# Optimization experiments

Measured on AMD Instinct MI355X. Metric: run time of the kernel, lower is better.

Reference implementation:

```python
import jax, jax.numpy as jnp
import numpy as np
from jax import lax

B, DIM, H, W = 4, 128, 128, 128
HEADS = 8
HID = int(DIM * 2.66)  # 340, IEL hidden_features
EPS_LN = 1e-6


def conv(x, w, b=None, groups=1, pad=0):
    out = lax.conv_general_dilated(
        x, w, (1, 1), [(pad, pad), (pad, pad)],
        feature_group_count=groups,
        dimension_numbers=('NCHW', 'OIHW', 'NCHW'))
    if b is not None:
        out = out + b[None, :, None, None]
    return out


def setup_inputs() -> dict:
    key = jax.random.key(0)
    ks = jax.random.split(key, 16)
    def wgt(k, shape, s=0.05):
        return jax.random.normal(k, shape, jnp.float32) * s
    return dict(
        x=jax.random.normal(ks[0], (B, DIM, H, W), jnp.float32),
        y=jax.random.normal(ks[1], (B, DIM, H, W), jnp.float32),
        ln_w=jnp.ones((DIM,), jnp.float32),
        ln_b=jnp.zeros((DIM,), jnp.float32),
        temperature=jnp.ones((HEADS, 1, 1), jnp.float32),
        q_w=wgt(ks[2], (DIM, DIM, 1, 1)),
        qdw_w=wgt(ks[3], (DIM, 1, 3, 3)),
        kv_w=wgt(ks[4], (2 * DIM, DIM, 1, 1)),
        kvdw_w=wgt(ks[5], (2 * DIM, 1, 3, 3)),
        po_w=wgt(ks[6], (DIM, DIM, 1, 1)),
        g1_w=wgt(ks[7], (DIM // 2, DIM, 1, 1)),
        g1_b=jnp.zeros((DIM // 2,), jnp.float32),
        g2_w=wgt(ks[8], (1, DIM // 2, 1, 1)),
        g2_b=jnp.zeros((1,), jnp.float32),
        pin_w=wgt(ks[9], (2 * HID, DIM, 1, 1)),
        dw_w=wgt(ks[10], (2 * HID, 1, 3, 3)),
        dw1_w=wgt(ks[11], (HID, 1, 3, 3)),
        dw2_w=wgt(ks[12], (HID, 1, 3, 3)),
        pout_w=wgt(ks[13], (DIM, HID, 1, 1)),
    )


def reference(x, y, ln_w, ln_b, temperature, q_w, qdw_w, kv_w, kvdw_w, po_w,
              g1_w, g1_b, g2_w, g2_b, pin_w, dw_w, dw1_w, dw2_w, pout_w):
    Bn, C, Hh, Ww = x.shape
    ch = C // HEADS  # channel tokens per head

    def ln(z):  # channels_first LayerNorm over channel axis
        u = z.mean(1, keepdims=True)
        s = ((z - u) ** 2).mean(1, keepdims=True)
        return ln_w[None, :, None, None] * ((z - u) / jnp.sqrt(s + EPS_LN)) + ln_b[None, :, None, None]

    xn = ln(x)
    yn = ln(y)

    # SCAB: transposed (channel) attention with dynamic top-k mask
    q = conv(conv(xn, q_w), qdw_w, groups=C, pad=1)
    kv = conv(conv(yn, kv_w), kvdw_w, groups=2 * C, pad=1)
    k, v = jnp.split(kv, 2, axis=1)
    q = q.reshape(Bn, HEADS, ch, Hh * Ww)
    k = k.reshape(Bn, HEADS, ch, Hh * Ww)
    v = v.reshape(Bn, HEADS, ch, Hh * Ww)
    q = q / jnp.maximum(jnp.linalg.norm(q, axis=-1, keepdims=True), 1e-12)
    k = k / jnp.maximum(jnp.linalg.norm(k, axis=-1, keepdims=True), 1e-12)

    # gate -> dynamic_k = int(ch * mean(gate)) as in torch (truncation)
    g = jax.nn.sigmoid(conv(jax.nn.relu(conv(xn, g1_w, g1_b)), g2_w, g2_b))
    dk = jnp.clip((ch * lax.stop_gradient(g).mean()).astype(jnp.int32), 1, ch)

    attn = jnp.einsum('bhcn,bhdn->bhcd', q, k) * temperature[None]  # [B,H,ch,ch]
    order = jnp.argsort(-attn, axis=-1)       # topk ordering (descending)
    ranks = jnp.argsort(order, axis=-1)       # rank of each entry in its row
    attn = jnp.where(ranks < dk, attn, -jnp.inf)
    attn = jax.nn.softmax(attn, axis=-1)
    out = jnp.einsum('bhcd,bhdn->bhcn', attn, v).reshape(Bn, C, Hh, Ww)
    x = x + conv(out, po_w)

    # IEL: tanh-gated dwconv FFN
    z = ln(x)
    t = conv(conv(z, pin_w), dw_w, groups=2 * HID, pad=1)
    x1, x2 = jnp.split(t, 2, axis=1)
    x1 = jnp.tanh(conv(x1, dw1_w, groups=HID, pad=1)) + x1
    x2 = jnp.tanh(conv(x2, dw2_w, groups=HID, pad=1)) + x2
    return conv(x1 * x2, pout_w) + x
```

## Files before the change

kernel.cpp:

```cpp
#include <hip/hip_runtime.h>
#include <math.h>

static constexpr int Bn    = 4;
static constexpr int Cc    = 128;
static constexpr int Hh    = 128;
static constexpr int Wb    = 128;
static constexpr int Nn    = Hh * Wb;
static constexpr int HEADS = 8;
static constexpr int CHh   = 16;
static constexpr int HID   = 340;
static constexpr int HID2  = 680;
static constexpr int NS    = 64;
static constexpr int MPAD  = 704;
static constexpr int KPAD2 = 352;

typedef unsigned short ushort_t;
typedef __attribute__((ext_vector_type(8))) short short8;
typedef __attribute__((ext_vector_type(4))) float f32x4;

__device__ __forceinline__ ushort_t f2bf(float f) {
    unsigned u = __float_as_uint(f);
    return (ushort_t)((u + 0x7FFFu + ((u >> 16) & 1u)) >> 16);
}
__device__ __forceinline__ float bf2f(ushort_t h) {
    return __uint_as_float(((unsigned)h) << 16);
}

__global__ __launch_bounds__(256) void ln_kernel(const float* __restrict__ in,
                                                 const float* __restrict__ w,
                                                 const float* __restrict__ bias,
                                                 float* __restrict__ out) {
    int p = blockIdx.x * 256 + threadIdx.x;
    int b = blockIdx.z;
    const float* ib = in + (size_t)b * Cc * Nn + p;
    float s = 0.f, s2 = 0.f;
    #pragma unroll 8
    for (int c = 0; c < Cc; ++c) {
        float v = ib[(size_t)c * Nn];
        s += v; s2 += v * v;
    }
    float mean = s * (1.0f / Cc);
    float var  = s2 * (1.0f / Cc) - mean * mean;
    float inv  = 1.0f / sqrtf(var + 1e-6f);
    float* ob = out + (size_t)b * Cc * Nn + p;
    #pragma unroll 8
    for (int c = 0; c < Cc; ++c) {
        float v = ib[(size_t)c * Nn];
        ob[(size_t)c * Nn] = w[c] * ((v - mean) * inv) + bias[c];
    }
}

__global__ __launch_bounds__(256) void ln_bf16_kernel(const float* __restrict__ in,
                                                      const float* __restrict__ w,
                                                      const float* __restrict__ bias,
                                                      ushort_t* __restrict__ out) {
    int p = blockIdx.x * 256 + threadIdx.x;
    int b = blockIdx.z;
    const float* ib = in + (size_t)b * Cc * Nn + p;
    float s = 0.f, s2 = 0.f;
    #pragma unroll 8
    for (int c = 0; c < Cc; ++c) {
        float v = ib[(size_t)c * Nn];
        s += v; s2 += v * v;
    }
    float mean = s * (1.0f / Cc);
    float var  = s2 * (1.0f / Cc) - mean * mean;
    float inv  = 1.0f / sqrtf(var + 1e-6f);
    ushort_t* ob = out + (size_t)b * Cc * Nn + p;
    #pragma unroll 8
    for (int c = 0; c < Cc; ++c) {
        float v = ib[(size_t)c * Nn];
        ob[(size_t)c * Nn] = f2bf(w[c] * ((v - mean) * inv) + bias[c]);
    }
}

__global__ __launch_bounds__(256) void wconv_pad_rows_kernel(const float* __restrict__ w,
                                                             ushort_t* __restrict__ o,
                                                             int rows, int K) {
    int idx = blockIdx.x * 256 + threadIdx.x;
    int r = idx / K, k = idx - r * K;
    o[idx] = (r < rows) ? f2bf(w[(size_t)r * K + k]) : (ushort_t)0;
}
__global__ __launch_bounds__(256) void wconv_pad_cols_kernel(const float* __restrict__ w,
                                                             ushort_t* __restrict__ o,
                                                             int K, int Kp) {
    int idx = blockIdx.x * 256 + threadIdx.x;
    int r = idx / Kp, k = idx - r * Kp;
    o[idx] = (k < K) ? f2bf(w[(size_t)r * K + k]) : (ushort_t)0;
}

__global__ __launch_bounds__(256) void gemm_bf16_kernel(const ushort_t* __restrict__ Zh,
                                                        const ushort_t* __restrict__ Wh,
                                                        const float* __restrict__ bias,
                                                        const float* __restrict__ res,
                                                        float* outf,
                                                        ushort_t* outh,
                                                        int Cin, int Kpad, int Mreal,
                                                        int act) {
    const int b    = blockIdx.z;
    const int px0  = blockIdx.x * 128;
    const int co0  = blockIdx.y * 64;
    const int tid  = threadIdx.x;
    const int wv   = tid >> 6;
    const int lane = tid & 63;
    const int n    = lane & 15;
    const int q    = lane >> 4;

    __shared__ ushort_t Bl[128][40];

    const ushort_t* Zb = Zh + (size_t)b * Cin * Nn;

    f32x4 acc[4][2];
    #pragma unroll
    for (int i = 0; i < 4; ++i)
        #pragma unroll
        for (int j = 0; j < 2; ++j) acc[i][j] = (f32x4){0.f, 0.f, 0.f, 0.f};

    for (int k0 = 0; k0 < Kpad; k0 += 32) {
        {
            int r = tid >> 3;
            int s = tid & 7;
            int ci = k0 + r;
            ushort_t tmp[16];
            if (ci < Cin) {
                const ushort_t* src = Zb + (size_t)ci * Nn + px0 + s * 16;
                uint4 v0 = *(const uint4*)src;
                uint4 v1 = *(const uint4*)(src + 8);
                tmp[0]  = (ushort_t)(v0.x & 0xFFFF); tmp[1]  = (ushort_t)(v0.x >> 16);
                tmp[2]  = (ushort_t)(v0.y & 0xFFFF); tmp[3]  = (ushort_t)(v0.y >> 16);
                tmp[4]  = (ushort_t)(v0.z & 0xFFFF); tmp[5]  = (ushort_t)(v0.z >> 16);
                tmp[6]  = (ushort_t)(v0.w & 0xFFFF); tmp[7]  = (ushort_t)(v0.w >> 16);
                tmp[8]  = (ushort_t)(v1.x & 0xFFFF); tmp[9]  = (ushort_t)(v1.x >> 16);
                tmp[10] = (ushort_t)(v1.y & 0xFFFF); tmp[11] = (ushort_t)(v1.y >> 16);
                tmp[12] = (ushort_t)(v1.z & 0xFFFF); tmp[13] = (ushort_t)(v1.z >> 16);
                tmp[14] = (ushort_t)(v1.w & 0xFFFF); tmp[15] = (ushort_t)(v1.w >> 16);
            } else {
                #pragma unroll
                for (int i = 0; i < 16; ++i) tmp[i] = 0;
            }
            #pragma unroll
            for (int i = 0; i < 16; ++i) Bl[s * 16 + i][r] = tmp[i];
        }
        __syncthreads();

        short8 bfrag[2];
        #pragma unroll
        for (int px16 = 0; px16 < 2; ++px16)
            bfrag[px16] = *(const short8*)&Bl[wv * 32 + px16 * 16 + n][q * 8];
        #pragma unroll
        for (int mt = 0; mt < 4; ++mt) {
            const ushort_t* wp = Wh + (size_t)(co0 + mt * 16 + n) * Kpad + k0 + q * 8;
            short8 afrag = *(const short8*)wp;
            #pragma unroll
            for (int px16 = 0; px16 < 2; ++px16)
                acc[mt][px16] = __builtin_amdgcn_mfma_f32_16x16x32_bf16(
                    afrag, bfrag[px16], acc[mt][px16], 0, 0, 0);
        }
        __syncthreads();
    }

    #pragma unroll
    for (int px16 = 0; px16 < 2; ++px16) {
        int px = px0 + wv * 32 + px16 * 16 + n;
        #pragma unroll
        for (int mt = 0; mt < 4; ++mt) {
            #pragma unroll
            for (int reg = 0; reg < 4; ++reg) {
                int co = co0 + mt * 16 + q * 4 + reg;
                if (co < Mreal) {
                    float v = acc[mt][px16][reg];
                    if (bias) v += bias[co];
                    if (act == 1) v = fmaxf(v, 0.f);
                    size_t o = ((size_t)b * Mreal + co) * Nn + px;
                    if (res)  v += res[o];
                    if (outf) outf[o] = v;
                    if (outh) outh[o] = f2bf(v);
                }
            }
        }
    }
}

template <int TCO>
__global__ __launch_bounds__(256) void conv1x1v_kernel(const float* __restrict__ in,
                                                       const float* __restrict__ wgt,
                                                       int wstride,
                                                       const float* __restrict__ bias,
                                                       const float* __restrict__ res,
                                                       float* __restrict__ out,
                                                       int Cin, int Cout, int act) {
    int pg  = blockIdx.x * 256 + threadIdx.x;
    int b   = blockIdx.z;
    int co0 = blockIdx.y * TCO;

    const float* wrow[TCO];
    #pragma unroll
    for (int i = 0; i < TCO; ++i) {
        int co = co0 + i; if (co > Cout - 1) co = Cout - 1;
        wrow[i] = wgt + (size_t)co * wstride;
    }

    float4 acc[TCO];
    #pragma unroll
    for (int i = 0; i < TCO; ++i) acc[i] = make_float4(0.f, 0.f, 0.f, 0.f);

    const float* ib = in + (size_t)b * Cin * Nn + (size_t)pg * 4;
    #pragma unroll 8
    for (int ci = 0; ci < Cin; ++ci) {
        float4 v = *(const float4*)(ib + (size_t)ci * Nn);
        #pragma unroll
        for (int i = 0; i < TCO; ++i) {
            float w = wrow[i][ci];
            acc[i].x += v.x * w; acc[i].y += v.y * w;
            acc[i].z += v.z * w; acc[i].w += v.w * w;
        }
    }

    #pragma unroll
    for (int i = 0; i < TCO; ++i) {
        int co = co0 + i;
        if (co < Cout) {
            float4 r = acc[i];
            if (bias) { float bb = bias[co]; r.x += bb; r.y += bb; r.z += bb; r.w += bb; }
            if (act == 1) {
                r.x = fmaxf(r.x, 0.f); r.y = fmaxf(r.y, 0.f);
                r.z = fmaxf(r.z, 0.f); r.w = fmaxf(r.w, 0.f);
            }
            size_t o = ((size_t)b * Cout + co) * Nn + (size_t)pg * 4;
            if (res) {
                float4 rv = *(const float4*)(res + o);
                r.x += rv.x; r.y += rv.y; r.z += rv.z; r.w += rv.w;
            }
            *(float4*)(out + o) = r;
        }
    }
}

__global__ __launch_bounds__(256) void dw3x3_kernel(const float* __restrict__ in,
                                                    const float* __restrict__ w,
                                                    float* __restrict__ out, int Ct) {
    int p = blockIdx.x * 256 + threadIdx.x;
    int c = blockIdx.y;
    int b = blockIdx.z;
    int y = p >> 7, x = p & (Wb - 1);
    const float* ib = in + ((size_t)b * Ct + c) * Nn;
    float wl[9];
    #pragma unroll
    for (int k = 0; k < 9; ++k) wl[k] = w[c * 9 + k];
    float acc = 0.f;
    #pragma unroll
    for (int dy = 0; dy < 3; ++dy) {
        int yy = y + dy - 1;
        if (yy < 0 || yy >= Hh) continue;
        #pragma unroll
        for (int dx = 0; dx < 3; ++dx) {
            int xx = x + dx - 1;
            if (xx < 0 || xx >= Wb) continue;
            acc += wl[dy * 3 + dx] * ib[yy * Wb + xx];
        }
    }
    out[((size_t)b * Ct + c) * Nn + p] = acc;
}

__global__ __launch_bounds__(256) void dw3x3_bf16_kernel(const ushort_t* __restrict__ in,
                                                         const float* __restrict__ w,
                                                         float* __restrict__ out, int Ct) {
    int p = blockIdx.x * 256 + threadIdx.x;
    int c = blockIdx.y;
    int b = blockIdx.z;
    int y = p >> 7, x = p & (Wb - 1);
    const ushort_t* ib = in + ((size_t)b * Ct + c) * Nn;
    float wl[9];
    #pragma unroll
    for (int k = 0; k < 9; ++k) wl[k] = w[c * 9 + k];
    float acc = 0.f;
    #pragma unroll
    for (int dy = 0; dy < 3; ++dy) {
        int yy = y + dy - 1;
        if (yy < 0 || yy >= Hh) continue;
        #pragma unroll
        for (int dx = 0; dx < 3; ++dx) {
            int xx = x + dx - 1;
            if (xx < 0 || xx >= Wb) continue;
            acc += wl[dy * 3 + dx] * bf2f(ib[yy * Wb + xx]);
        }
    }
    out[((size_t)b * Ct + c) * Nn + p] = acc;
}

__global__ __launch_bounds__(256) void l2norm_kernel(float* __restrict__ data, int cstride) {
    int b = blockIdx.z, c = blockIdx.x;
    float* ptr = data + ((size_t)b * cstride + c) * Nn;
    int t = threadIdx.x;
    float s = 0.f;
    for (int i = t; i < Nn; i += 256) { float v = ptr[i]; s += v * v; }
    __shared__ float red[256];
    red[t] = s; __syncthreads();
    for (int st = 128; st > 0; st >>= 1) { if (t < st) red[t] += red[t + st]; __syncthreads(); }
    float scale = 1.0f / fmaxf(sqrtf(red[0]), 1e-12f);
    for (int i = t; i < Nn; i += 256) ptr[i] *= scale;
}

__global__ __launch_bounds__(256) void gate2_kernel(const float* __restrict__ gmid,
                                                    const float* __restrict__ w2,
                                                    const float* __restrict__ b2,
                                                    float* __restrict__ blocksums,
                                                    int out_off) {
    int p = blockIdx.x * 256 + threadIdx.x;
    int b = blockIdx.z;
    float acc = b2[0];
    const float* ib = gmid + (size_t)b * 64 * Nn + p;
    #pragma unroll 8
    for (int ci = 0; ci < 64; ++ci) acc += ib[(size_t)ci * Nn] * w2[ci];
    float g = 1.0f / (1.0f + expf(-acc));
    __shared__ float red[256];
    int t = threadIdx.x;
    red[t] = g; __syncthreads();
    for (int st = 128; st > 0; st >>= 1) { if (t < st) red[t] += red[t + st]; __syncthreads(); }
    if (t == 0) blocksums[out_off + b * 64 + blockIdx.x] = red[0];
}

__global__ __launch_bounds__(256) void gate_final_kernel(const float* __restrict__ blocksums,
                                                         int* __restrict__ dk_out) {
    __shared__ double sred[256];
    int t = threadIdx.x;
    sred[t] = (double)blocksums[t];
    __syncthreads();
    for (int st = 128; st > 0; st >>= 1) { if (t < st) sred[t] += sred[t + st]; __syncthreads(); }
    if (t == 0) {
        double mean = sred[0] / (double)(Bn * Nn);
        float val = 16.0f * (float)mean;
        int dk = (int)val;
        if (dk < 1) dk = 1;
        if (dk > 16) dk = 16;
        *dk_out = dk;
    }
}

__global__ __launch_bounds__(256) void attn_qk_partial_kernel(const float* __restrict__ q,
                                                              const float* __restrict__ k,
                                                              int kstride,
                                                              float* __restrict__ partial) {
    int ns = blockIdx.x, h = blockIdx.y, b = blockIdx.z;
    int t = threadIdx.x;
    int c = t >> 4, d = t & 15;
    __shared__ float qs[16][65];
    __shared__ float ks[16][65];
    const float* qb = q + ((size_t)b * Cc + h * CHh) * Nn;
    const float* kb = k + ((size_t)b * kstride + h * CHh) * Nn;
    float acc = 0.f;
    int nbeg = ns * (Nn / NS);
    for (int n0 = nbeg; n0 < nbeg + (Nn / NS); n0 += 64) {
        for (int idx = t; idx < 1024; idx += 256) {
            int r = idx >> 6, col = idx & 63;
            qs[r][col] = qb[(size_t)r * Nn + n0 + col];
            ks[r][col] = kb[(size_t)r * Nn + n0 + col];
        }
        __syncthreads();
        #pragma unroll
        for (int j = 0; j < 64; ++j) acc += qs[c][j] * ks[d][j];
        __syncthreads();
    }
    partial[(((size_t)(b * HEADS + h)) * NS + ns) * 256 + t] = acc;
}

__global__ __launch_bounds__(256) void attn_reduce_kernel(const float* __restrict__ partial,
                                                          const float* __restrict__ temp,
                                                          float* __restrict__ attnp) {
    int bh = blockIdx.x;
    int h = bh % HEADS;
    int t = threadIdx.x;
    const float* pp = partial + (size_t)bh * NS * 256 + t;
    float s = 0.f;
    #pragma unroll 8
    for (int ns = 0; ns < NS; ++ns) s += pp[(size_t)ns * 256];
    attnp[(size_t)bh * 256 + t] = s * temp[h];
}

__global__ void topk_softmax_kernel(float* __restrict__ attnp, const int* __restrict__ dkp) {
    int bh = blockIdx.x;
    int c = threadIdx.x;
    if (c >= 16) return;
    float* row = attnp + ((size_t)bh * CHh + c) * CHh;
    float a[16];
    #pragma unroll
    for (int d = 0; d < 16; ++d) a[d] = row[d];
    int dk = *dkp;
    unsigned keep = 0;
    float m = -INFINITY;
    #pragma unroll
    for (int d = 0; d < 16; ++d) {
        int rank = 0;
        #pragma unroll
        for (int j = 0; j < 16; ++j)
            rank += (a[j] > a[d]) || (a[j] == a[d] && j < d);
        if (rank < dk) { keep |= (1u << d); m = fmaxf(m, a[d]); }
    }
    float e[16]; float s = 0.f;
    #pragma unroll
    for (int d = 0; d < 16; ++d) {
        e[d] = (keep >> d & 1u) ? expf(a[d] - m) : 0.f;
        s += e[d];
    }
    float invs = 1.0f / s;
    #pragma unroll
    for (int d = 0; d < 16; ++d) row[d] = e[d] * invs;
}

__global__ __launch_bounds__(256) void attn_v_kernel(const float* __restrict__ attnp,
                                                     const float* __restrict__ v,
                                                     float* __restrict__ out) {
    int p = blockIdx.x * 256 + threadIdx.x;
    int cg = blockIdx.y;
    int b = blockIdx.z;
    int h = cg >> 4, cr = cg & 15;
    const float* arow = attnp + (((size_t)b * HEADS + h) * CHh + cr) * CHh;
    const float* vb = v + ((size_t)b * Cc + h * CHh) * Nn + p;
    float acc = 0.f;
    #pragma unroll
    for (int d = 0; d < 16; ++d) acc += arow[d] * vb[(size_t)d * Nn];
    out[((size_t)b * Cc + cg) * Nn + p] = acc;
}

__global__ __launch_bounds__(256) void attn_v_bf16_kernel(const float* __restrict__ attnp,
                                                          const float* __restrict__ v,
                                                          int vstride, int voff,
                                                          ushort_t* __restrict__ out) {
    int p = blockIdx.x * 256 + threadIdx.x;
    int cg = blockIdx.y;
    int b = blockIdx.z;
    int h = cg >> 4, cr = cg & 15;
    const float* arow = attnp + (((size_t)b * HEADS + h) * CHh + cr) * CHh;
    const float* vb = v + ((size_t)b * vstride + voff + h * CHh) * Nn + p;
    float acc = 0.f;
    #pragma unroll
    for (int d = 0; d < 16; ++d) acc += arow[d] * vb[(size_t)d * Nn];
    out[((size_t)b * Cc + cg) * Nn + p] = f2bf(acc);
}

__global__ __launch_bounds__(256) void iel_tail_v4_kernel(const ushort_t* __restrict__ Th,
                                                          const float* __restrict__ dww,
                                                          const float* __restrict__ dw1p,
                                                          const float* __restrict__ dw2p,
                                                          ushort_t* __restrict__ PRh) {
    const int gy0 = blockIdx.x * 16;
    const int c   = blockIdx.y;
    const int b   = blockIdx.z;
    const int tid = threadIdx.x;

    __shared__ float ts[2][20][132];
    __shared__ float us[2][18][132];

    const ushort_t* t1 = Th + ((size_t)b * HID2 + c) * Nn;
    const ushort_t* t2 = Th + ((size_t)b * HID2 + HID + c) * Nn;

    for (int idx = tid; idx < 640; idx += 256) {
        int ti  = idx / 320;
        int rem = idx - ti * 320;
        int i   = rem >> 4;
        int seg = rem & 15;
        int gy  = gy0 - 2 + i;
        const ushort_t* tp = ti ? t2 : t1;
        float vals[8];
        if (gy >= 0 && gy < Hh) {
            uint4 v = *(const uint4*)(tp + gy * Wb + seg * 8);
            vals[0] = bf2f((ushort_t)(v.x & 0xFFFF)); vals[1] = bf2f((ushort_t)(v.x >> 16));
            vals[2] = bf2f((ushort_t)(v.y & 0xFFFF)); vals[3] = bf2f((ushort_t)(v.y >> 16));
            vals[4] = bf2f((ushort_t)(v.z & 0xFFFF)); vals[5] = bf2f((ushort_t)(v.z >> 16));
            vals[6] = bf2f((ushort_t)(v.w & 0xFFFF)); vals[7] = bf2f((ushort_t)(v.w >> 16));
        } else {
            #pragma unroll
            for (int k = 0; k < 8; ++k) vals[k] = 0.f;
        }
        #pragma unroll
        for (int k = 0; k < 8; ++k) ts[ti][i][1 + seg * 8 + k] = vals[k];
        if (seg == 0)  ts[ti][i][0] = 0.f;
        if (seg == 15) { ts[ti][i][129] = 0.f; ts[ti][i][130] = 0.f; ts[ti][i][131] = 0.f; }
    }
    __syncthreads();

    float wA[9], wB[9], w1[9], w2[9];
    #pragma unroll
    for (int k = 0; k < 9; ++k) {
        wA[k] = dww[c * 9 + k];
        wB[k] = dww[(HID + c) * 9 + k];
        w1[k] = dw1p[c * 9 + k];
        w2[k] = dw2p[c * 9 + k];
    }

    for (int idx = tid; idx < 1152; idx += 256) {
        int ti  = idx / 576;
        int rem = idx - ti * 576;
        int i   = rem >> 5;
        int s   = rem & 31;
        int gy  = gy0 - 1 + i;
        float o0 = 0.f, o1 = 0.f, o2 = 0.f, o3 = 0.f;
        if (gy >= 0 && gy < Hh) {
            const float* wp = ti ? wB : wA;
            #pragma unroll
            for (int dy = 0; dy < 3; ++dy) {
                const float* row = &ts[ti][i + dy][4 * s];
                float4 a = *(const float4*)row;
                float2 bb = *(const float2*)(row + 4);
                float w0 = wp[dy * 3 + 0], w1t = wp[dy * 3 + 1], w2t = wp[dy * 3 + 2];
                o0 += w0 * a.x + w1t * a.y + w2t * a.z;
                o1 += w0 * a.y + w1t * a.z + w2t * a.w;
                o2 += w0 * a.z + w1t * a.w + w2t * bb.x;
                o3 += w0 * a.w + w1t * bb.x + w2t * bb.y;
            }
        }
        int j0 = 1 + 4 * s;
        us[ti][i][j0]     = o0;
        us[ti][i][j0 + 1] = o1;
        us[ti][i][j0 + 2] = o2;
        us[ti][i][j0 + 3] = o3;
    }
    if (tid < 72) {
        int ti = tid / 36;
        int r  = tid - ti * 36;
        int i  = r >> 1;
        us[ti][i][(r & 1) ? 129 : 0] = 0.f;
    }
    __syncthreads();

    ushort_t* outp = PRh + ((size_t)b * HID + c) * Nn;
    for (int idx = tid; idx < 512; idx += 256) {
        int r  = idx >> 5;
        int s  = idx & 31;
        int x0 = 4 * s;
        float s1a[4] = {0.f, 0.f, 0.f, 0.f};
        float s2a[4] = {0.f, 0.f, 0.f, 0.f};
        float c1a[4], c2a[4];
        #pragma unroll
        for (int dy = 0; dy < 3; ++dy) {
            const float* r0 = &us[0][r + dy][x0];
            float4 a0 = *(const float4*)r0;
            float2 b0 = *(const float2*)(r0 + 4);
            const float* r1 = &us[1][r + dy][x0];
            float4 a1 = *(const float4*)r1;
            float2 b1 = *(const float2*)(r1 + 4);
            float w10 = w1[dy * 3], w11 = w1[dy * 3 + 1], w12 = w1[dy * 3 + 2];
            float w20 = w2[dy * 3], w21 = w2[dy * 3 + 1], w22 = w2[dy * 3 + 2];
            s1a[0] += w10 * a0.x + w11 * a0.y + w12 * a0.z;
            s1a[1] += w10 * a0.y + w11 * a0.z + w12 * a0.w;
            s1a[2] += w10 * a0.z + w11 * a0.w + w12 * b0.x;
            s1a[3] += w10 * a0.w + w11 * b0.x + w12 * b0.y;
            s2a[0] += w20 * a1.x + w21 * a1.y + w22 * a1.z;
            s2a[1] += w20 * a1.y + w21 * a1.z + w22 * a1.w;
            s2a[2] += w20 * a1.z + w21 * a1.w + w22 * b1.x;
            s2a[3] += w20 * a1.w + w21 * b1.x + w22 * b1.y;
            if (dy == 1) {
                c1a[0] = a0.y; c1a[1] = a0.z; c1a[2] = a0.w; c1a[3] = b0.x;
                c2a[0] = a1.y; c2a[1] = a1.z; c2a[2] = a1.w; c2a[3] = b1.x;
            }
        }
        uint2 pk;
        float v0 = (tanhf(s1a[0]) + c1a[0]) * (tanhf(s2a[0]) + c2a[0]);
        float v1 = (tanhf(s1a[1]) + c1a[1]) * (tanhf(s2a[1]) + c2a[1]);
        float v2 = (tanhf(s1a[2]) + c1a[2]) * (tanhf(s2a[2]) + c2a[2]);
        float v3 = (tanhf(s1a[3]) + c1a[3]) * (tanhf(s2a[3]) + c2a[3]);
        pk.x = (unsigned)f2bf(v0) | ((unsigned)f2bf(v1) << 16);
        pk.y = (unsigned)f2bf(v2) | ((unsigned)f2bf(v3) << 16);
        *(uint2*)(outp + (gy0 + r) * Wb + x0) = pk;
    }
}

__global__ __launch_bounds__(256) void iel_tail_f32_kernel(const float* __restrict__ t1p,
                                                           const float* __restrict__ t2p,
                                                           const float* __restrict__ dwA,
                                                           const float* __restrict__ dwB,
                                                           const float* __restrict__ dw1p,
                                                           const float* __restrict__ dw2p,
                                                           float* __restrict__ prod) {
    const int c = blockIdx.y;
    const int tilesx = Wb / 16;
    const int ty0 = (blockIdx.x / tilesx) * 16;
    const int tx0 = (blockIdx.x % tilesx) * 16;
    const int tid = threadIdx.x;

    __shared__ float ts[2][20][24];
    __shared__ float us[2][18][24];

    const float* t1 = t1p + (size_t)c * Nn;
    const float* t2 = t2p + (size_t)c * Nn;

    for (int idx = tid; idx < 400; idx += 256) {
        int i = idx / 20, j = idx % 20;
        int gy = ty0 - 2 + i, gx = tx0 - 2 + j;
        bool ok = (gy >= 0 && gy < Hh && gx >= 0 && gx < Wb);
        ts[0][i][j] = ok ? t1[gy * Wb + gx] : 0.f;
        ts[1][i][j] = ok ? t2[gy * Wb + gx] : 0.f;
    }
    __syncthreads();

    float wA[9], wB[9], w1[9], w2[9];
    #pragma unroll
    for (int k = 0; k < 9; ++k) {
        wA[k] = dwA[c * 9 + k];
        wB[k] = dwB[c * 9 + k];
        w1[k] = dw1p[c * 9 + k];
        w2[k] = dw2p[c * 9 + k];
    }

    for (int idx = tid; idx < 324; idx += 256) {
        int i = idx / 18, j = idx % 18;
        int gy = ty0 - 1 + i, gx = tx0 - 1 + j;
        float a0 = 0.f, a1 = 0.f;
        if (gy >= 0 && gy < Hh && gx >= 0 && gx < Wb) {
            #pragma unroll
            for (int dy = 0; dy < 3; ++dy)
                #pragma unroll
                for (int dx = 0; dx < 3; ++dx) {
                    a0 += wA[dy * 3 + dx] * ts[0][i + dy][j + dx];
                    a1 += wB[dy * 3 + dx] * ts[1][i + dy][j + dx];
                }
        }
        us[0][i][j] = a0;
        us[1][i][j] = a1;
    }
    __syncthreads();

    int ty = tid >> 4, tx = tid & 15;
    float c1 = us[0][ty + 1][tx + 1];
    float c2 = us[1][ty + 1][tx + 1];
    float s1 = 0.f, s2 = 0.f;
    #pragma unroll
    for (int dy = 0; dy < 3; ++dy)
        #pragma unroll
        for (int dx = 0; dx < 3; ++dx) {
            s1 += w1[dy * 3 + dx] * us[0][ty + dy][tx + dx];
            s2 += w2[dy * 3 + dx] * us[1][ty + dy][tx + dx];
        }
    float x1t = tanhf(s1) + c1;
    float x2t = tanhf(s2) + c2;
    prod[(size_t)c * Nn + (ty0 + ty) * Wb + (tx0 + tx)] = x1t * x2t;
}

extern "C" void kernel_launch(void* const* d_in, const int* in_sizes, int n_in,
                              void* d_out, int out_size, void* d_ws, size_t ws_size,
                              hipStream_t stream) {
    const float* x      = (const float*)d_in[0];
    const float* y      = (const float*)d_in[1];
    const float* ln_w   = (const float*)d_in[2];
    const float* ln_b   = (const float*)d_in[3];
    const float* temp   = (const float*)d_in[4];
    const float* q_w    = (const float*)d_in[5];
    const float* qdw_w  = (const float*)d_in[6];
    const float* kv_w   = (const float*)d_in[7];
    const float* kvdw_w = (const float*)d_in[8];
    const float* po_w   = (const float*)d_in[9];
    const float* g1_w   = (const float*)d_in[10];
    const float* g1_b   = (const float*)d_in[11];
    const float* g2_w   = (const float*)d_in[12];
    const float* g2_b   = (const float*)d_in[13];
    const float* pin_w  = (const float*)d_in[14];
    const float* dw_w   = (const float*)d_in[15];
    const float* dw1_w  = (const float*)d_in[16];
    const float* dw2_w  = (const float*)d_in[17];
    const float* pout_w = (const float*)d_in[18];
    float* out = (float*)d_out;

    char* ws = (char*)d_ws;
    float* attn      = (float*)ws;
    float* blocksums = (float*)(ws + 32768);
    int*   dk        = (int*)(ws + 33792);
    ushort_t* qWh  = (ushort_t*)(ws + 34816);
    ushort_t* kvWh = qWh + 16384;
    ushort_t* poWh = kvWh + 32768;
    ushort_t* g1Wh = poWh + 16384;
    ushort_t* Wh1  = g1Wh + 8192;
    ushort_t* Wh2  = Wh1 + (size_t)MPAD * Cc;
    float* pool    = (float*)(ws + (1u << 20));

    const size_t CN    = (size_t)Cc * Nn;
    const size_t SLOT1 = (size_t)Bn * CN;
    const size_t TIER1_NEED = 65536 + 6 * SLOT1 * 4;

    dim3 blk(256);
    const int PGX = Nn / 1024;

    if (ws_size >= TIER1_NEED) {
        float* S3 = pool;
        float* S4 = pool + 8 * 1024 * 1024;
        ushort_t* XNh  = (ushort_t*)(pool + 24 * 1024 * 1024);
        ushort_t* YNh  = XNh + Bn * CN;
        ushort_t* KV1h = YNh + Bn * CN;
        ushort_t* Q1h  = KV1h + 2 * Bn * CN;
        float* gmid    = (float*)Q1h;
        float* partial = gmid;
        ushort_t* AOh  = XNh;

        wconv_pad_rows_kernel<<<dim3(64), blk, 0, stream>>>(q_w, qWh, 128, Cc);
        wconv_pad_rows_kernel<<<dim3(128), blk, 0, stream>>>(kv_w, kvWh, 256, Cc);
        wconv_pad_rows_kernel<<<dim3(64), blk, 0, stream>>>(po_w, poWh, 128, Cc);
        wconv_pad_rows_kernel<<<dim3(32), blk, 0, stream>>>(g1_w, g1Wh, 64, Cc);
        wconv_pad_rows_kernel<<<dim3(MPAD * Cc / 256), blk, 0, stream>>>(pin_w, Wh1, HID2, Cc);
        wconv_pad_cols_kernel<<<dim3(Cc * KPAD2 / 256), blk, 0, stream>>>(pout_w, Wh2, HID, KPAD2);

        ln_bf16_kernel<<<dim3(Nn / 256, 1, Bn), blk, 0, stream>>>(x, ln_w, ln_b, XNh);
        ln_bf16_kernel<<<dim3(Nn / 256, 1, Bn), blk, 0, stream>>>(y, ln_w, ln_b, YNh);

        gemm_bf16_kernel<<<dim3(Nn / 128, 2, Bn), blk, 0, stream>>>(
            XNh, qWh, nullptr, nullptr, nullptr, Q1h, Cc, Cc, Cc, 0);
        dw3x3_bf16_kernel<<<dim3(Nn / 256, Cc, Bn), blk, 0, stream>>>(Q1h, qdw_w, S3, Cc);

        gemm_bf16_kernel<<<dim3(Nn / 128, 4, Bn), blk, 0, stream>>>(
            YNh, kvWh, nullptr, nullptr, nullptr, KV1h, Cc, Cc, 2 * Cc, 0);
        dw3x3_bf16_kernel<<<dim3(Nn / 256, 2 * Cc, Bn), blk, 0, stream>>>(KV1h, kvdw_w, S4, 2 * Cc);

        gemm_bf16_kernel<<<dim3(Nn / 128, 1, Bn), blk, 0, stream>>>(
            XNh, g1Wh, g1_b, nullptr, gmid, nullptr, Cc, Cc, 64, 1);
        gate2_kernel<<<dim3(Nn / 256, 1, Bn), blk, 0, stream>>>(gmid, g2_w, g2_b, blocksums, 0);
        gate_final_kernel<<<dim3(1), blk, 0, stream>>>(blocksums, dk);

        l2norm_kernel<<<dim3(Cc, 1, Bn), blk, 0, stream>>>(S3, Cc);
        l2norm_kernel<<<dim3(Cc, 1, Bn), blk, 0, stream>>>(S4, 2 * Cc);

        attn_qk_partial_kernel<<<dim3(NS, HEADS, Bn), blk, 0, stream>>>(S3, S4, 2 * Cc, partial);
        attn_reduce_kernel<<<dim3(Bn * HEADS), blk, 0, stream>>>(partial, temp, attn);
        topk_softmax_kernel<<<dim3(Bn * HEADS), dim3(16), 0, stream>>>(attn, dk);
        attn_v_bf16_kernel<<<dim3(Nn / 256, Cc, Bn), blk, 0, stream>>>(
            attn, S4, 2 * Cc, Cc, AOh);

        gemm_bf16_kernel<<<dim3(Nn / 128, 2, Bn), blk, 0, stream>>>(
            AOh, poWh, nullptr, x, out, nullptr, Cc, Cc, Cc, 0);

        ushort_t* ZNh = (ushort_t*)pool;
        ushort_t* Th  = ZNh + Bn * CN;
        ushort_t* PRh = Th + (size_t)Bn * HID2 * Nn;

        ln_bf16_kernel<<<dim3(Nn / 256, 1, Bn), blk, 0, stream>>>(out, ln_w, ln_b, ZNh);

        gemm_bf16_kernel<<<dim3(Nn / 128, MPAD / 64, Bn), blk, 0, stream>>>(
            ZNh, Wh1, nullptr, nullptr, nullptr, Th, Cc, Cc, HID2, 0);

        iel_tail_v4_kernel<<<dim3(Hh / 16, HID, Bn), blk, 0, stream>>>(
            Th, dw_w, dw1_w, dw2_w, PRh);

        gemm_bf16_kernel<<<dim3(Nn / 128, 2, Bn), blk, 0, stream>>>(
            PRh, Wh2, nullptr, out, out, nullptr, HID, KPAD2, Cc, 0);
    } else {
        float* s0 = pool;
        float* s1 = pool + 1 * CN;
        float* s2 = pool + 2 * CN;
        float* s3 = pool + 3 * CN;
        float* s4 = pool + 4 * CN;
        float* s5 = pool + 5 * CN;

        for (int b = 0; b < Bn; ++b) {
            const float* xb = x + (size_t)b * CN;
            ln_kernel<<<dim3(Nn / 256, 1, 1), blk, 0, stream>>>(xb, ln_w, ln_b, s0);
            conv1x1v_kernel<4><<<dim3(PGX, 16, 1), blk, 0, stream>>>(
                s0, g1_w, Cc, g1_b, nullptr, s1, Cc, 64, 1);
            gate2_kernel<<<dim3(Nn / 256, 1, 1), blk, 0, stream>>>(
                s1, g2_w, g2_b, blocksums, b * 64);
        }
        gate_final_kernel<<<dim3(1), blk, 0, stream>>>(blocksums, dk);

        for (int b = 0; b < Bn; ++b) {
            const float* xb = x + (size_t)b * CN;
            const float* yb = y + (size_t)b * CN;
            float* outb = out + (size_t)b * CN;
            float* attnb = attn + (size_t)b * HEADS * CHh * CHh;

            ln_kernel<<<dim3(Nn / 256, 1, 1), blk, 0, stream>>>(xb, ln_w, ln_b, s0);
            ln_kernel<<<dim3(Nn / 256, 1, 1), blk, 0, stream>>>(yb, ln_w, ln_b, s1);

            conv1x1v_kernel<8><<<dim3(PGX, 16, 1), blk, 0, stream>>>(
                s0, q_w, Cc, nullptr, nullptr, s2, Cc, Cc, 0);
            dw3x3_kernel<<<dim3(Nn / 256, Cc, 1), blk, 0, stream>>>(s2, qdw_w, s3, Cc);
            l2norm_kernel<<<dim3(Cc, 1, 1), blk, 0, stream>>>(s3, Cc);

            conv1x1v_kernel<8><<<dim3(PGX, 16, 1), blk, 0, stream>>>(
                s1, kv_w, Cc, nullptr, nullptr, s2, Cc, Cc, 0);
            dw3x3_kernel<<<dim3(Nn / 256, Cc, 1), blk, 0, stream>>>(s2, kvdw_w, s4, Cc);
            l2norm_kernel<<<dim3(Cc, 1, 1), blk, 0, stream>>>(s4, Cc);

            conv1x1v_kernel<8><<<dim3(PGX, 16, 1), blk, 0, stream>>>(
                s1, kv_w + 128 * 128, Cc, nullptr, nullptr, s2, Cc, Cc, 0);
            dw3x3_kernel<<<dim3(Nn / 256, Cc, 1), blk, 0, stream>>>(s2, kvdw_w + 128 * 9, s5, Cc);

            attn_qk_partial_kernel<<<dim3(NS, HEADS, 1), blk, 0, stream>>>(s3, s4, Cc, s2);
            attn_reduce_kernel<<<dim3(HEADS), blk, 0, stream>>>(s2, temp, attnb);
            topk_softmax_kernel<<<dim3(HEADS), dim3(16), 0, stream>>>(attnb, dk);
            attn_v_kernel<<<dim3(Nn / 256, Cc, 1), blk, 0, stream>>>(attnb, s5, s2);

            conv1x1v_kernel<8><<<dim3(PGX, 16, 1), blk, 0, stream>>>(
                s2, po_w, Cc, nullptr, xb, outb, Cc, Cc, 0);
        }

        const int CHUNK = 170;
        const size_t TCH = (size_t)CHUNK * Nn;
        float* zn   = pool;
        float* T1   = pool + CN;
        float* T2   = T1 + TCH;
        float* prod = T2 + TCH;
        for (int b = 0; b < Bn; ++b) {
            float* outb = out + (size_t)b * CN;
            ln_kernel<<<dim3(Nn / 256, 1, 1), blk, 0, stream>>>(outb, ln_w, ln_b, zn);
            for (int c0 = 0; c0 < HID; c0 += CHUNK) {
                conv1x1v_kernel<20><<<dim3(PGX, 9, 1), blk, 0, stream>>>(
                    zn, pin_w + (size_t)c0 * Cc, Cc, nullptr, nullptr, T1, Cc, CHUNK, 0);
                conv1x1v_kernel<20><<<dim3(PGX, 9, 1), blk, 0, stream>>>(
                    zn, pin_w + (size_t)(HID + c0) * Cc, Cc, nullptr, nullptr, T2, Cc, CHUNK, 0);
                iel_tail_f32_kernel<<<dim3(64, CHUNK, 1), blk, 0, stream>>>(
                    T1, T2, dw_w + c0 * 9, dw_w + (HID + c0) * 9,
                    dw1_w + c0 * 9, dw2_w + c0 * 9, prod);
                conv1x1v_kernel<8><<<dim3(PGX, 16, 1), blk, 0, stream>>>(
                    prod, pout_w + c0, HID, nullptr, outb, outb, CHUNK, Cc, 0);
            }
        }
    }
}
```

Baseline: 719.0 us.

## Fold L2 normalization into dwconv sum-of-squares and rescale attention logits

The depthwise 3x3 conv for q and kv is rewritten to stage rows in shared memory, produce four outputs per thread with vector stores, and accumulate per-channel sums of squares through atomics. The two separate l2norm passes over q and k are removed; the norms are applied instead as a scale on the 16x16 attention logits in the reduce kernel. The IEL tail also swaps tanhf for a fast exp/rcp tanh. The cost is atomic float accumulation, which is order-dependent, and slightly lower tanh accuracy.

```diff
diff --git a/kernel.cpp b/kernel.cpp
--- a/kernel.cpp
+++ b/kernel.cpp
@@ -26,6 +26,38 @@
     return __uint_as_float(((unsigned)h) << 16);
 }
 
+__device__ __forceinline__ float fast_tanh(float x) {
+    float a = fabsf(x);
+    a = fminf(a, 12.0f);
+    float e = __expf(2.0f * a);
+    float r = 1.0f - 2.0f * __builtin_amdgcn_rcpf(e + 1.0f);
+    return x < 0.0f ? -r : r;
+}
+
+__device__ __forceinline__ void iel7_stage(float (*ts)[136], const ushort_t* __restrict__ tp,
+                                           int gy0, int tid) {
+    for (int idx = tid; idx < 640; idx += 256) {
+        int i = idx >> 5;
+        int s = idx & 31;
+        int gy = gy0 - 2 + i;
+        float4 v; v.x = 0.f; v.y = 0.f; v.z = 0.f; v.w = 0.f;
+        if (gy >= 0 && gy < Hh) {
+            uint2 u = *(const uint2*)(tp + gy * Wb + 4 * s);
+            v.x = bf2f((ushort_t)(u.x & 0xFFFF)); v.y = bf2f((ushort_t)(u.x >> 16));
+            v.z = bf2f((ushort_t)(u.y & 0xFFFF)); v.w = bf2f((ushort_t)(u.y >> 16));
+        }
+        *(float4*)&ts[i][4 + 4 * s] = v;
+        if (s == 0) {
+            float4 z; z.x = 0.f; z.y = 0.f; z.z = 0.f; z.w = 0.f;
+            *(float4*)&ts[i][0] = z;
+        }
+        if (s == 31) {
+            float4 z; z.x = 0.f; z.y = 0.f; z.z = 0.f; z.w = 0.f;
+            *(float4*)&ts[i][132] = z;
+        }
+    }
+}
+
 __global__ __launch_bounds__(256) void ln_kernel(const float* __restrict__ in,
                                                  const float* __restrict__ w,
                                                  const float* __restrict__ bias,
@@ -87,6 +119,11 @@
     int idx = blockIdx.x * 256 + threadIdx.x;
     int r = idx / Kp, k = idx - r * Kp;
     o[idx] = (k < K) ? f2bf(w[(size_t)r * K + k]) : (ushort_t)0;
+}
+
+__global__ __launch_bounds__(256) void zero_f32_kernel(float* __restrict__ p, int n) {
+    int i = blockIdx.x * 256 + threadIdx.x;
+    if (i < n) p[i] = 0.f;
 }
 
 __global__ __launch_bounds__(256) void gemm_bf16_kernel(const ushort_t* __restrict__ Zh,
@@ -262,30 +299,57 @@
     out[((size_t)b * Ct + c) * Nn + p] = acc;
 }
 
-__global__ __launch_bounds__(256) void dw3x3_bf16_kernel(const ushort_t* __restrict__ in,
-                                                         const float* __restrict__ w,
-                                                         float* __restrict__ out, int Ct) {
-    int p = blockIdx.x * 256 + threadIdx.x;
-    int c = blockIdx.y;
-    int b = blockIdx.z;
-    int y = p >> 7, x = p & (Wb - 1);
+__global__ __launch_bounds__(256) void dw3x3_bf16_v3_kernel(const ushort_t* __restrict__ in,
+                                                            const float* __restrict__ w,
+                                                            float* __restrict__ out, int Ct,
+                                                            float* __restrict__ ssq,
+                                                            int nrmC) {
+    const int gy0 = blockIdx.x * 16;
+    const int c   = blockIdx.y;
+    const int b   = blockIdx.z;
+    const int tid = threadIdx.x;
+
+    __shared__ float ts[20][136];
+
     const ushort_t* ib = in + ((size_t)b * Ct + c) * Nn;
+    iel7_stage(ts, ib, gy0, tid);
+    __syncthreads();
+
     float wl[9];
     #pragma unroll
     for (int k = 0; k < 9; ++k) wl[k] = w[c * 9 + k];
-    float acc = 0.f;
-    #pragma unroll
-    for (int dy = 0; dy < 3; ++dy) {
-        int yy = y + dy - 1;
-        if (yy < 0 || yy >= Hh) continue;
-        #pragma unroll
-        for (int dx = 0; dx < 3; ++dx) {
-            int xx = x + dx - 1;
-            if (xx < 0 || xx >= Wb) continue;
-            acc += wl[dy * 3 + dx] * bf2f(ib[yy * Wb + xx]);
-        }
-    }
-    out[((size_t)b * Ct + c) * Nn + p] = acc;
+
+    float* ob = out + ((size_t)b * Ct + c) * Nn;
+    float s2sum = 0.f;
+    #pragma unroll
+    for (int it = 0; it < 2; ++it) {
+        int idx = tid + it * 256;
+        int r = idx >> 5;
+        int s = idx & 31;
+        float a[4] = {0.f, 0.f, 0.f, 0.f};
+        #pragma unroll
+        for (int dy = 0; dy < 3; ++dy) {
+            const float* row = &ts[r + 1 + dy][4 * s];
+            float4 e0 = *(const float4*)row;
+            float4 e1 = *(const float4*)(row + 4);
+            float4 e2 = *(const float4*)(row + 8);
+            float e[12] = {e0.x, e0.y, e0.z, e0.w, e1.x, e1.y, e1.z, e1.w,
+                           e2.x, e2.y, e2.z, e2.w};
+            float w0 = wl[dy * 3], w1 = wl[dy * 3 + 1], w2 = wl[dy * 3 + 2];
+            #pragma unroll
+            for (int p = 0; p < 4; ++p)
+                a[p] += w0 * e[p + 3] + w1 * e[p + 4] + w2 * e[p + 5];
+        }
+        float4 st; st.x = a[0]; st.y = a[1]; st.z = a[2]; st.w = a[3];
+        *(float4*)(ob + (gy0 + r) * Wb + 4 * s) = st;
+        s2sum += a[0] * a[0] + a[1] * a[1] + a[2] * a[2] + a[3] * a[3];
+    }
+
+    if (ssq != nullptr && c < nrmC) {
+        #pragma unroll
+        for (int o = 32; o > 0; o >>= 1) s2sum += __shfl_xor(s2sum, o, 64);
+        if ((tid & 63) == 0) atomicAdd(&ssq[(size_t)b * nrmC + c], s2sum);
+    }
 }
 
 __global__ __launch_bounds__(256) void l2norm_kernel(float* __restrict__ data, int cstride) {
@@ -320,8 +384,8 @@
     if (t == 0) blocksums[out_off + b * 64 + blockIdx.x] = red[0];
 }
 
-__global__ __launch_bounds__(256) void gate_final_kernel(const float* __restrict__ blocksums,
-                                                         int* __restrict__ dk_out) {
+__global__ void gate_final_kernel(const float* __restrict__ blocksums,
+                                  int* __restrict__ dk_out) {
     __shared__ double sred[256];
     int t = threadIdx.x;
     sred[t] = (double)blocksums[t];
@@ -366,6 +430,8 @@
 
 __global__ __launch_bounds__(256) void attn_reduce_kernel(const float* __restrict__ partial,
                                                           const float* __restrict__ temp,
+                                                          const float* __restrict__ qss,
+                                                          const float* __restrict__ kss,
                                                           float* __restrict__ attnp) {
     int bh = blockIdx.x;
     int h = bh % HEADS;
@@ -374,7 +440,16 @@
     float s = 0.f;
     #pragma unroll 8
     for (int ns = 0; ns < NS; ++ns) s += pp[(size_t)ns * 256];
-    attnp[(size_t)bh * 256 + t] = s * temp[h];
+    float scale = temp[h];
+    if (qss != nullptr) {
+        int b  = bh / HEADS;
+        int cQ = h * CHh + (t >> 4);
+        int cK = h * CHh + (t & 15);
+        float nq = fmaxf(sqrtf(qss[(size_t)b * Cc + cQ]), 1e-12f);
+        float nk = fmaxf(sqrtf(kss[(size_t)b * Cc + cK]), 1e-12f);
+        scale = scale / (nq * nk);
+    }
+    attnp[(size_t)bh * 256 + t] = s * scale;
 }
 
 __global__ void topk_softmax_kernel(float* __restrict__ attnp, const int* __restrict__ dkp) {
@@ -555,10 +630,10 @@
             }
         }
         uint2 pk;
-        float v0 = (tanhf(s1a[0]) + c1a[0]) * (tanhf(s2a[0]) + c2a[0]);
-        float v1 = (tanhf(s1a[1]) + c1a[1]) * (tanhf(s2a[1]) + c2a[1]);
-        float v2 = (tanhf(s1a[2]) + c1a[2]) * (tanhf(s2a[2]) + c2a[2]);
-        float v3 = (tanhf(s1a[3]) + c1a[3]) * (tanhf(s2a[3]) + c2a[3]);
+        float v0 = (fast_tanh(s1a[0]) + c1a[0]) * (fast_tanh(s2a[0]) + c2a[0]);
+        float v1 = (fast_tanh(s1a[1]) + c1a[1]) * (fast_tanh(s2a[1]) + c2a[1]);
+        float v2 = (fast_tanh(s1a[2]) + c1a[2]) * (fast_tanh(s2a[2]) + c2a[2]);
+        float v3 = (fast_tanh(s1a[3]) + c1a[3]) * (fast_tanh(s2a[3]) + c2a[3]);
         pk.x = (unsigned)f2bf(v0) | ((unsigned)f2bf(v1) << 16);
         pk.y = (unsigned)f2bf(v2) | ((unsigned)f2bf(v3) << 16);
         *(uint2*)(outp + (gy0 + r) * Wb + x0) = pk;
@@ -670,6 +745,8 @@
     ushort_t* g1Wh = poWh + 16384;
     ushort_t* Wh1  = g1Wh + 8192;
     ushort_t* Wh2  = Wh1 + (size_t)MPAD * Cc;
+    float* qss = (float*)(ws + 458752);
+    float* kss = (float*)(ws + 460800);
     float* pool    = (float*)(ws + (1u << 20));
 
     const size_t CN    = (size_t)Cc * Nn;
@@ -696,28 +773,28 @@
         wconv_pad_rows_kernel<<<dim3(32), blk, 0, stream>>>(g1_w, g1Wh, 64, Cc);
         wconv_pad_rows_kernel<<<dim3(MPAD * Cc / 256), blk, 0, stream>>>(pin_w, Wh1, HID2, Cc);
         wconv_pad_cols_kernel<<<dim3(Cc * KPAD2 / 256), blk, 0, stream>>>(pout_w, Wh2, HID, KPAD2);
+        zero_f32_kernel<<<dim3(4), blk, 0, stream>>>(qss, 2 * Bn * Cc);
 
         ln_bf16_kernel<<<dim3(Nn / 256, 1, Bn), blk, 0, stream>>>(x, ln_w, ln_b, XNh);
         ln_bf16_kernel<<<dim3(Nn / 256, 1, Bn), blk, 0, stream>>>(y, ln_w, ln_b, YNh);
 
         gemm_bf16_kernel<<<dim3(Nn / 128, 2, Bn), blk, 0, stream>>>(
             XNh, qWh, nullptr, nullptr, nullptr, Q1h, Cc, Cc, Cc, 0);
-        dw3x3_bf16_kernel<<<dim3(Nn / 256, Cc, Bn), blk, 0, stream>>>(Q1h, qdw_w, S3, Cc);
+        dw3x3_bf16_v3_kernel<<<dim3(Hh / 16, Cc, Bn), blk, 0, stream>>>(
+            Q1h, qdw_w, S3, Cc, qss, Cc);
 
         gemm_bf16_kernel<<<dim3(Nn / 128, 4, Bn), blk, 0, stream>>>(
             YNh, kvWh, nullptr, nullptr, nullptr, KV1h, Cc, Cc, 2 * Cc, 0);
-        dw3x3_bf16_kernel<<<dim3(Nn / 256, 2 * Cc, Bn), blk, 0, stream>>>(KV1h, kvdw_w, S4, 2 * Cc);
+        dw3x3_bf16_v3_kernel<<<dim3(Hh / 16, 2 * Cc, Bn), blk, 0, stream>>>(
+            KV1h, kvdw_w, S4, 2 * Cc, kss, Cc);
 
         gemm_bf16_kernel<<<dim3(Nn / 128, 1, Bn), blk, 0, stream>>>(
             XNh, g1Wh, g1_b, nullptr, gmid, nullptr, Cc, Cc, 64, 1);
         gate2_kernel<<<dim3(Nn / 256, 1, Bn), blk, 0, stream>>>(gmid, g2_w, g2_b, blocksums, 0);
         gate_final_kernel<<<dim3(1), blk, 0, stream>>>(blocksums, dk);
 
-        l2norm_kernel<<<dim3(Cc, 1, Bn), blk, 0, stream>>>(S3, Cc);
-        l2norm_kernel<<<dim3(Cc, 1, Bn), blk, 0, stream>>>(S4, 2 * Cc);
-
         attn_qk_partial_kernel<<<dim3(NS, HEADS, Bn), blk, 0, stream>>>(S3, S4, 2 * Cc, partial);
-        attn_reduce_kernel<<<dim3(Bn * HEADS), blk, 0, stream>>>(partial, temp, attn);
+        attn_reduce_kernel<<<dim3(Bn * HEADS), blk, 0, stream>>>(partial, temp, qss, kss, attn);
         topk_softmax_kernel<<<dim3(Bn * HEADS), dim3(16), 0, stream>>>(attn, dk);
         attn_v_bf16_kernel<<<dim3(Nn / 256, Cc, Bn), blk, 0, stream>>>(
             attn, S4, 2 * Cc, Cc, AOh);
@@ -781,7 +858,7 @@
             dw3x3_kernel<<<dim3(Nn / 256, Cc, 1), blk, 0, stream>>>(s2, kvdw_w + 128 * 9, s5, Cc);
 
             attn_qk_partial_kernel<<<dim3(NS, HEADS, 1), blk, 0, stream>>>(s3, s4, Cc, s2);
-            attn_reduce_kernel<<<dim3(HEADS), blk, 0, stream>>>(s2, temp, attnb);
+            attn_reduce_kernel<<<dim3(HEADS), blk, 0, stream>>>(s2, temp, nullptr, nullptr, attnb);
             topk_softmax_kernel<<<dim3(HEADS), dim3(16), 0, stream>>>(attnb, dk);
             attn_v_kernel<<<dim3(Nn / 256, Cc, 1), blk, 0, stream>>>(attnb, s5, s2);
 
```

Result: faster. 629.0 us (-12.5%).
